# Performance work log

Hardware: AMD Instinct MI355X
Metric: run time of the kernel (lower is better)

Reference implementation:

```python
import jax, jax.numpy as jnp
import numpy as np

# ---- static configuration (mirrors init_kwargs) ----
B, V, C, NH, HD = 1, 6, 256, 8, 32     # batch, views, embed, heads, head_dim
Z, L, P = 4, 4, 2                       # z-ref points, fmap levels, ref points
BEV_H, BEV_W = 80, 80
Q = BEV_H * BEV_W
IMG_H, IMG_W = 480, 800
LEVEL_SHAPES = [(60, 100), (30, 50), (15, 25), (8, 13)]
S = sum(h * w for h, w in LEVEL_SHAPES)
RES = 0.512
OFFSET_SCALE = 1.0
FF = 512


def layer_norm(x, g, b):
    m = jnp.mean(x, -1, keepdims=True)
    v = jnp.var(x, -1, keepdims=True)
    return (x - m) / jnp.sqrt(v + 1e-5) * g + b


def _bev_grid():
    xs = (jnp.arange(BEV_W) + 0.5) / BEV_W
    ys = (jnp.arange(BEV_H) + 0.5) / BEV_H
    gy, gx = jnp.meshgrid(ys, xs, indexing='ij')
    ref = jnp.stack([gx.reshape(-1), gy.reshape(-1)], -1)        # (Q,2) normalized xy
    world = (ref - 0.5) * jnp.array([BEV_W * RES, BEV_H * RES])  # (Q,2) ego-frame meters
    return ref, world


def deform_sample(value, H, W, loc):
    """Bilinear sampling. value: (N, H*W, NH, HD); loc: (N, Qn, NH, PP, 2) in [0,1].
    Returns (N, Qn, NH, PP, HD); out-of-bounds samples contribute zero."""
    v = jnp.moveaxis(value, 2, 1)                                # (N, NH, HW, HD)
    x = loc[..., 0] * W - 0.5
    y = loc[..., 1] * H - 0.5
    x0 = jnp.floor(x); y0 = jnp.floor(y)
    lx, ly = x - x0, y - y0
    x0 = x0.astype(jnp.int32); y0 = y0.astype(jnp.int32)
    gather = jax.vmap(jax.vmap(lambda vt, it: vt[it]))           # over (N, NH)
    def corner(xi, yi, w):
        ok = ((xi >= 0) & (xi < W) & (yi >= 0) & (yi < H)).astype(value.dtype)
        idx = jnp.clip(yi, 0, H - 1) * W + jnp.clip(xi, 0, W - 1)
        g = gather(v, jnp.moveaxis(idx, 2, 1))                   # (N,NH,Qn,PP,HD)
        return jnp.moveaxis(g, 1, 2) * (w * ok)[..., None]
    return (corner(x0, y0, (1 - lx) * (1 - ly)) + corner(x0 + 1, y0, lx * (1 - ly))
            + corner(x0, y0 + 1, (1 - lx) * ly) + corner(x0 + 1, y0 + 1, lx * ly))


def _forward(bev_queries, bev_histories, multiscale_fmaps, transition_matrices, z_refs,
             cam_proj_matrices, Wv_t, Woff_t, boff_t, Ww_t, bw_t, Wo_t, bo_t, ln1_g, ln1_b,
             Wv_s, Woff_s, boff_s, Ww_s, bw_s, Wo_s, bo_s, ln2_g, ln2_b,
             W1, b1, W2, b2, ln3_g, ln3_b):
    ref, world = _bev_grid()
    q = bev_queries
    # ---------- temporal self-attention (deformable over current + warped history) ----------
    vcur = (q @ Wv_t).reshape(B, Q, NH, HD)
    vhist = (bev_histories @ Wv_t).reshape(B, Q, NH, HD)
    off_t = (q @ Woff_t + boff_t).reshape(B, Q, NH, 2, P, 2) * OFFSET_SCALE
    w_t = jax.nn.softmax((q @ Ww_t + bw_t).reshape(B, Q, NH, 2 * P), -1).reshape(B, Q, NH, 2, P)
    ext = jnp.array([BEV_W * RES, BEV_H * RES], jnp.float32)
    wh = jnp.concatenate([world, jnp.ones((Q, 1), jnp.float32)], -1)     # (Q,3)
    warped = jnp.einsum('bij,qj->bqi', transition_matrices, wh)          # (B,Q,3)
    ref_hist = warped[..., :2] / warped[..., 2:3] / ext + 0.5            # (B,Q,2)
    norm_bev = jnp.array([BEV_W, BEV_H], jnp.float32)
    loc_c = ref[None, :, None, None, :] + off_t[:, :, :, 0] / norm_bev
    loc_h = ref_hist[:, :, None, None, :] + off_t[:, :, :, 1] / norm_bev
    s_c = deform_sample(vcur, BEV_H, BEV_W, loc_c)                       # (B,Q,NH,P,HD)
    s_h = deform_sample(vhist, BEV_H, BEV_W, loc_h)
    out_t = (jnp.einsum('bqhp,bqhpd->bqhd', w_t[:, :, :, 0], s_c)
             + jnp.einsum('bqhp,bqhpd->bqhd', w_t[:, :, :, 1], s_h))
    out1 = out_t.reshape(B, Q, C) @ Wo_t + bo_t
    out2 = layer_norm(out1 + q, ln1_g, ln1_b)
    # ---------- spatial cross-attention (multi-view multi-scale deformable) ----------
    val = (multiscale_fmaps @ Wv_s).reshape(B * V, S, NH, HD)
    pts = jnp.concatenate([
        jnp.broadcast_to(world[:, None, :], (Q, Z, 2)),
        jnp.broadcast_to(z_refs[None, :, None], (Q, Z, 1)),
        jnp.ones((Q, Z, 1), jnp.float32)], -1)                           # (Q,Z,4) homogeneous
    uvd = jnp.einsum('vij,qzj->vqzi', cam_proj_matrices, pts)            # (V,Q,Z,3)
    d = uvd[..., 2]
    un = uvd[..., 0] / jnp.maximum(d, 1e-5) / IMG_W
    vn = uvd[..., 1] / jnp.maximum(d, 1e-5) / IMG_H
    valid = ((d > 1e-5) & (un >= 0) & (un <= 1) & (vn >= 0) & (vn <= 1)).astype(q.dtype)
    refuv = jnp.stack([un, vn], -1)                                      # (V,Q,Z,2)
    off_s = (out2 @ Woff_s + boff_s).reshape(B, Q, NH, Z, L, P, 2) * OFFSET_SCALE
    w_s = jax.nn.softmax((out2 @ Ww_s + bw_s).reshape(B, Q, NH, Z * L * P), -1)
    w_s = w_s.reshape(B, Q, NH, Z, L, P)
    acc = jnp.zeros((B, Q, NH, HD), q.dtype)
    start = 0
    for l, (Hl, Wl) in enumerate(LEVEL_SHAPES):
        vl = val[:, start:start + Hl * Wl]
        start += Hl * Wl
        loc = (refuv[None, :, :, None, :, None, :]
               + off_s[:, None, :, :, :, l] / jnp.array([Wl, Hl], jnp.float32))
        loc = jnp.broadcast_to(loc, (B, V, Q, NH, Z, P, 2)).reshape(B * V, Q, NH, Z * P, 2)
        samp = deform_sample(vl, Hl, Wl, loc).reshape(B, V, Q, NH, Z, P, HD)
        wl = w_s[:, None, :, :, :, l] * valid[None, :, :, None, :, None]
        acc = acc + jnp.einsum('bvqhzp,bvqhzpd->bqhd', wl, samp)
    count = jnp.maximum(valid.sum((0, 2)), 1.0)                          # (Q,) hit count
    out3 = (acc / count[None, :, None, None]).reshape(B, Q, C) @ Wo_s + bo_s
    out4 = layer_norm(out3 + out2, ln2_g, ln2_b)
    # ---------- feed-forward ----------
    out5 = jax.nn.relu(out4 @ W1 + b1) @ W2 + b2
    return layer_norm(out5 + out4, ln3_g, ln3_b)


def setup_inputs() -> dict:
    key = jax.random.key(0)
    ks = iter(jax.random.split(key, 40))
    def rn(shape, s=1.0):
        return jax.random.normal(next(ks), shape, jnp.float32) * s
    sc = 1.0 / float(np.sqrt(C))
    inp = {}
    inp['bev_queries'] = rn((B, Q, C), 0.1)
    inp['bev_histories'] = rn((B, Q, C), 0.1)
    inp['multiscale_fmaps'] = rn((B, V, S, C), 0.1)
    th = 0.02
    T = np.array([[np.cos(th), -np.sin(th), 0.5],
                  [np.sin(th), np.cos(th), 0.1],
                  [0.0, 0.0, 1.0]], np.float32)
    inp['transition_matrices'] = jnp.tile(jnp.asarray(T)[None], (B, 1, 1))
    inp['z_refs'] = jnp.linspace(-5.0, 3.0, Z).astype(jnp.float32)
    K = np.array([[400.0, 0.0, IMG_W / 2], [0.0, 400.0, IMG_H / 2], [0.0, 0.0, 1.0]], np.float32)
    Ps = []
    for vi in range(V):
        a = 2 * np.pi * vi / V
        Rt = np.zeros((3, 4), np.float32)
        Rt[0, :3] = [-np.sin(a), np.cos(a), 0.0]   # camera right
        Rt[1, :3] = [0.0, 0.0, -1.0]               # camera down
        Rt[2, :3] = [np.cos(a), np.sin(a), 0.0]    # camera forward
        Ps.append(K @ Rt)
    inp['cam_proj_matrices'] = jnp.asarray(np.stack(Ps))
    # temporal self-attention params
    inp['Wv_t'] = rn((C, C), sc)
    inp['Woff_t'] = rn((C, NH * 2 * P * 2), sc * 0.1)
    inp['boff_t'] = jnp.zeros((NH * 2 * P * 2,), jnp.float32)
    inp['Ww_t'] = rn((C, NH * 2 * P), sc)
    inp['bw_t'] = jnp.zeros((NH * 2 * P,), jnp.float32)
    inp['Wo_t'] = rn((C, C), sc)
    inp['bo_t'] = jnp.zeros((C,), jnp.float32)
    inp['ln1_g'] = jnp.ones((C,), jnp.float32)
    inp['ln1_b'] = jnp.zeros((C,), jnp.float32)
    # spatial cross-attention params
    inp['Wv_s'] = rn((C, C), sc)
    inp['Woff_s'] = rn((C, NH * Z * L * P * 2), sc * 0.1)
    inp['boff_s'] = jnp.zeros((NH * Z * L * P * 2,), jnp.float32)
    inp['Ww_s'] = rn((C, NH * Z * L * P), sc)
    inp['bw_s'] = jnp.zeros((NH * Z * L * P,), jnp.float32)
    inp['Wo_s'] = rn((C, C), sc)
    inp['bo_s'] = jnp.zeros((C,), jnp.float32)
    inp['ln2_g'] = jnp.ones((C,), jnp.float32)
    inp['ln2_b'] = jnp.zeros((C,), jnp.float32)
    # FFN params
    inp['W1'] = rn((C, FF), sc)
    inp['b1'] = jnp.zeros((FF,), jnp.float32)
    inp['W2'] = rn((FF, C), 1.0 / float(np.sqrt(FF)))
    inp['b2'] = jnp.zeros((C,), jnp.float32)
    inp['ln3_g'] = jnp.ones((C,), jnp.float32)
    inp['ln3_b'] = jnp.zeros((C,), jnp.float32)
    # static shape descriptors (treated as compile-time constants)
    inp['bev_spatial_shape'] = np.array([[BEV_H, BEV_W]], np.int64)
    inp['multiscale_fmap_shapes'] = np.array(LEVEL_SHAPES, np.int64)
    inp['img_spatial_shape'] = np.array([[IMG_H, IMG_W]], np.int64)
    return inp


def reference(bev_queries, bev_histories, multiscale_fmaps, transition_matrices, z_refs,
              cam_proj_matrices, Wv_t, Woff_t, boff_t, Ww_t, bw_t, Wo_t, bo_t, ln1_g, ln1_b,
              Wv_s, Woff_s, boff_s, Ww_s, bw_s, Wo_s, bo_s, ln2_g, ln2_b,
              W1, b1, W2, b2, ln3_g, ln3_b,
              bev_spatial_shape, multiscale_fmap_shapes, img_spatial_shape):
    return _forward(bev_queries, bev_histories, multiscale_fmaps, transition_matrices, z_refs,
                    cam_proj_matrices, Wv_t, Woff_t, boff_t, Ww_t, bw_t, Wo_t, bo_t, ln1_g, ln1_b,
                    Wv_s, Woff_s, boff_s, Ww_s, bw_s, Wo_s, bo_s, ln2_g, ln2_b,
                    W1, b1, W2, b2, ln3_g, ln3_b)
```

## Files before the change

kernel.cpp:

```cpp
#include <hip/hip_runtime.h>
#include <hip/hip_bf16.h>
#include <hip/hip_fp16.h>

typedef unsigned short u16;
typedef unsigned int u32;
typedef __attribute__((ext_vector_type(8))) short bf16x8;
typedef __attribute__((ext_vector_type(4))) float f32x4;

#define Q_N  6400
#define S_N  7979
#define BEV  80

__device__ __forceinline__ float ubf(u16 u) {
    return __uint_as_float(((u32)u) << 16);
}
__device__ __forceinline__ u16 bfrn(float x) {
    u32 b = __float_as_uint(x);
    return (u16)((b + 0x7FFFu + ((b >> 16) & 1u)) >> 16);
}
__device__ __forceinline__ float f16tof(u16 u) {
    __half h; *(u16*)&h = u; return __half2float(h);
}
__device__ __forceinline__ u16 ftof16(float f) {
    __half h = __float2half(f); return *(u16*)&h;
}

template <int AIN, int RELU, int OUTMODE, int SM4, int SM32>
__device__ __forceinline__ void gemm_body(
    const void* __restrict__ A, const u16* __restrict__ WhT, const u16* __restrict__ WlT,
    const float* __restrict__ bias, const float* __restrict__ bias2,
    void* __restrict__ Cout, int M, int N, int K, int bx, int by,
    u16* Ah, u16* Al, u16* Wh, u16* Wl)
{
    const int tid  = threadIdx.x;
    const int lane = tid & 63;
    const int wave = tid >> 6;
    const int wm = (wave >> 1) * 32, wn = (wave & 1) * 64;
    const int m0 = by * 64, n0 = bx * 128;
    const int arow = tid >> 2, ak = (tid & 3) * 8;
    const int wrow = tid >> 1, wk = (tid & 1) * 16;
    const int fr = lane & 15, g = lane >> 4;

    f32x4 acc[8];
    #pragma unroll
    for (int i = 0; i < 8; ++i) acc[i] = (f32x4)(0.f);

    for (int k0 = 0; k0 < K; k0 += 32) {
        {
            const bool okr = (m0 + arow) < M;
            float vals[8];
            if (AIN == 0) {
                const float* ap = (const float*)A + (size_t)(m0 + arow) * K + k0 + ak;
                float4 v0 = okr ? *(const float4*)(ap)     : make_float4(0.f, 0.f, 0.f, 0.f);
                float4 v1 = okr ? *(const float4*)(ap + 4) : make_float4(0.f, 0.f, 0.f, 0.f);
                vals[0] = v0.x; vals[1] = v0.y; vals[2] = v0.z; vals[3] = v0.w;
                vals[4] = v1.x; vals[5] = v1.y; vals[6] = v1.z; vals[7] = v1.w;
            } else {
                const u16* ap = (const u16*)A + (size_t)(m0 + arow) * K + k0 + ak;
                uint4 u = okr ? *(const uint4*)ap : make_uint4(0, 0, 0, 0);
                const __half2* hp = (const __half2*)&u;
                #pragma unroll
                for (int i = 0; i < 4; ++i) {
                    float2 f = __half22float2(hp[i]);
                    vals[2 * i] = f.x; vals[2 * i + 1] = f.y;
                }
            }
            u16 hb[8], lb[8];
            #pragma unroll
            for (int i = 0; i < 8; ++i) {
                hb[i] = bfrn(vals[i]);
                lb[i] = bfrn(vals[i] - ubf(hb[i]));
            }
            u16* dh = &Ah[arow * 40 + ak];
            u16* dl = &Al[arow * 40 + ak];
            *(ushort4*)(dh)     = *(ushort4*)&hb[0];
            *(ushort4*)(dh + 4) = *(ushort4*)&hb[4];
            *(ushort4*)(dl)     = *(ushort4*)&lb[0];
            *(ushort4*)(dl + 4) = *(ushort4*)&lb[4];
        }
        {
            const size_t wo = (size_t)(n0 + wrow) * K + k0 + wk;
            *(uint4*)&Wh[wrow * 40 + wk]     = *(const uint4*)(WhT + wo);
            *(uint4*)&Wh[wrow * 40 + wk + 8] = *(const uint4*)(WhT + wo + 8);
            *(uint4*)&Wl[wrow * 40 + wk]     = *(const uint4*)(WlT + wo);
            *(uint4*)&Wl[wrow * 40 + wk + 8] = *(const uint4*)(WlT + wo + 8);
        }
        __syncthreads();
        bf16x8 fah[2], fal[2], fwh[4], fwl[4];
        #pragma unroll
        for (int i = 0; i < 2; ++i) {
            fah[i] = *(const bf16x8*)&Ah[(wm + i * 16 + fr) * 40 + g * 8];
            fal[i] = *(const bf16x8*)&Al[(wm + i * 16 + fr) * 40 + g * 8];
        }
        #pragma unroll
        for (int j = 0; j < 4; ++j) {
            fwh[j] = *(const bf16x8*)&Wh[(wn + j * 16 + fr) * 40 + g * 8];
            fwl[j] = *(const bf16x8*)&Wl[(wn + j * 16 + fr) * 40 + g * 8];
        }
        #pragma unroll
        for (int i = 0; i < 2; ++i)
            #pragma unroll
            for (int j = 0; j < 4; ++j) {
                acc[i * 4 + j] = __builtin_amdgcn_mfma_f32_16x16x32_bf16(fah[i], fwh[j], acc[i * 4 + j], 0, 0, 0);
                acc[i * 4 + j] = __builtin_amdgcn_mfma_f32_16x16x32_bf16(fal[i], fwh[j], acc[i * 4 + j], 0, 0, 0);
                acc[i * 4 + j] = __builtin_amdgcn_mfma_f32_16x16x32_bf16(fah[i], fwl[j], acc[i * 4 + j], 0, 0, 0);
            }
        __syncthreads();
    }
    const int g4r = g * 4;
    float bv[4];
    #pragma unroll
    for (int j = 0; j < 4; ++j) {
        int col = n0 + wn + j * 16 + fr;
        if (bias2) bv[j] = (col < 512) ? bias[col] : bias2[col - 512];
        else       bv[j] = bias ? bias[col] : 0.f;
    }
    const bool do_sm32 = SM32 && ((n0 + wn) >= 512);
    const bool do_sm4  = SM4 && (wn == 64);
    #pragma unroll
    for (int i = 0; i < 2; ++i) {
        #pragma unroll
        for (int r = 0; r < 4; ++r) {
            const int row = m0 + wm + i * 16 + g4r + r;
            float v0 = acc[i * 4 + 0][r] + bv[0];
            float v1 = acc[i * 4 + 1][r] + bv[1];
            float v2 = acc[i * 4 + 2][r] + bv[2];
            float v3 = acc[i * 4 + 3][r] + bv[3];
            if (RELU) {
                v0 = fmaxf(v0, 0.f); v1 = fmaxf(v1, 0.f);
                v2 = fmaxf(v2, 0.f); v3 = fmaxf(v3, 0.f);
            }
            if (SM4 && do_sm4) {
                float m0q = fmaxf(v0, __shfl_xor(v0, 1));
                m0q = fmaxf(m0q, __shfl_xor(m0q, 2));
                float e0 = __expf(v0 - m0q);
                float s0 = e0 + __shfl_xor(e0, 1);
                s0 += __shfl_xor(s0, 2);
                v0 = e0 / s0;
                float m1q = fmaxf(v1, __shfl_xor(v1, 1));
                m1q = fmaxf(m1q, __shfl_xor(m1q, 2));
                float e1 = __expf(v1 - m1q);
                float s1 = e1 + __shfl_xor(e1, 1);
                s1 += __shfl_xor(s1, 2);
                v1 = e1 / s1;
                v2 = 0.f; v3 = 0.f;
            }
            if (SM32 && do_sm32) {
                float ma = fmaxf(v0, v1);
                ma = fmaxf(ma, __shfl_xor(ma, 1));
                ma = fmaxf(ma, __shfl_xor(ma, 2));
                ma = fmaxf(ma, __shfl_xor(ma, 4));
                ma = fmaxf(ma, __shfl_xor(ma, 8));
                float e0 = __expf(v0 - ma), e1 = __expf(v1 - ma);
                float sa = e0 + e1;
                sa += __shfl_xor(sa, 1);
                sa += __shfl_xor(sa, 2);
                sa += __shfl_xor(sa, 4);
                sa += __shfl_xor(sa, 8);
                float ia = 1.f / sa;
                v0 = e0 * ia; v1 = e1 * ia;
                float mb = fmaxf(v2, v3);
                mb = fmaxf(mb, __shfl_xor(mb, 1));
                mb = fmaxf(mb, __shfl_xor(mb, 2));
                mb = fmaxf(mb, __shfl_xor(mb, 4));
                mb = fmaxf(mb, __shfl_xor(mb, 8));
                float e2 = __expf(v2 - mb), e3 = __expf(v3 - mb);
                float sb = e2 + e3;
                sb += __shfl_xor(sb, 1);
                sb += __shfl_xor(sb, 2);
                sb += __shfl_xor(sb, 4);
                sb += __shfl_xor(sb, 8);
                float ib = 1.f / sb;
                v2 = e2 * ib; v3 = e3 * ib;
            }
            if (row < M) {
                const int colb = n0 + wn + fr;
                if (OUTMODE == 1) {
                    u16* cp = (u16*)Cout + (size_t)row * N;
                    cp[colb]      = ftof16(v0);
                    cp[colb + 16] = ftof16(v1);
                    cp[colb + 32] = ftof16(v2);
                    cp[colb + 48] = ftof16(v3);
                } else {
                    float* cp = (float*)Cout + (size_t)row * N;
                    cp[colb]      = v0;
                    cp[colb + 16] = v1;
                    cp[colb + 32] = v2;
                    cp[colb + 48] = v3;
                }
            }
        }
    }
}

template <int AIN, int RELU, int OUTMODE, int SM32>
__global__ __launch_bounds__(256) void mgemm_k(
    const void* __restrict__ A, const u16* __restrict__ WhT, const u16* __restrict__ WlT,
    const float* __restrict__ bias, const float* __restrict__ bias2,
    void* __restrict__ Cout, int M, int N, int K)
{
    __shared__ u16 Ah[64 * 40], Al[64 * 40], Wh[128 * 40], Wl[128 * 40];
    gemm_body<AIN, RELU, OUTMODE, 0, SM32>(A, WhT, WlT, bias, bias2, Cout,
                                           M, N, K, blockIdx.x, blockIdx.y, Ah, Al, Wh, Wl);
}

__global__ __launch_bounds__(256) void fused3_k(
    const float* __restrict__ fmaps, const float* __restrict__ q, const float* __restrict__ hist,
    const u16* __restrict__ Wv_s_h, const u16* __restrict__ Wv_s_l,
    const u16* __restrict__ Wv_t_h, const u16* __restrict__ Wv_t_l,
    const u16* __restrict__ Wc_h,   const u16* __restrict__ Wc_l,
    const float* __restrict__ bc,
    u16* __restrict__ val_f16, u16* __restrict__ vcur, u16* __restrict__ vhist,
    float* __restrict__ owt)
{
    __shared__ u16 Ah[64 * 40], Al[64 * 40], Wh[128 * 40], Wl[128 * 40];
    const int b = blockIdx.x;
    if (b < 1498) {
        gemm_body<0, 0, 1, 0, 0>(fmaps, Wv_s_h, Wv_s_l, nullptr, nullptr, val_f16,
                                 47874, 256, 256, b & 1, b >> 1, Ah, Al, Wh, Wl);
    } else if (b < 1698) {
        int l = b - 1498;
        gemm_body<0, 0, 1, 0, 0>(q, Wv_t_h, Wv_t_l, nullptr, nullptr, vcur,
                                 6400, 256, 256, l & 1, l >> 1, Ah, Al, Wh, Wl);
    } else if (b < 1898) {
        int l = b - 1698;
        gemm_body<0, 0, 1, 0, 0>(hist, Wv_t_h, Wv_t_l, nullptr, nullptr, vhist,
                                 6400, 256, 256, l & 1, l >> 1, Ah, Al, Wh, Wl);
    } else {
        int l = b - 1898;
        gemm_body<0, 0, 0, 1, 0>(q, Wc_h, Wc_l, bc, nullptr, owt,
                                 6400, 128, 256, 0, l, Ah, Al, Wh, Wl);
    }
}

__global__ __launch_bounds__(256) void wprep_k(
    const float* __restrict__ w0, const float* __restrict__ w1, const float* __restrict__ w2,
    const float* __restrict__ w3, const float* __restrict__ w4, const float* __restrict__ w5,
    const float* __restrict__ w6, const float* __restrict__ w7, u16* __restrict__ base,
    const float* __restrict__ Woff_t, const float* __restrict__ Ww_t,
    const float* __restrict__ boff_t, const float* __restrict__ bw_t,
    float* __restrict__ bc)
{
    const int b = blockIdx.x, tid = threadIdx.x;
    if (b == 184) {
        if (tid < 128) bc[tid] = (tid < 64) ? boff_t[tid] : (tid < 96 ? bw_t[tid - 64] : 0.f);
        return;
    }
    const int cum[10]  = {0, 16, 32, 48, 80, 96, 112, 144, 176, 184};
    const int Ks[9]    = {256, 256, 256, 256, 256, 256, 256, 512, 256};
    const int Ns[9]    = {256, 256, 256, 512, 256, 256, 512, 256, 128};
    const int hoff[9]  = {0, 131072, 262144, 393216, 524288, 786432, 917504, 1179648, 1441792};
    const int loff[9]  = {65536, 196608, 327680, 589824, 720896, 851968, 1048576, 1310720, 1474560};
    int seg = 0;
    #pragma unroll
    for (int s = 1; s < 9; ++s) if (b >= cum[s]) seg = s;
    const int K = Ks[seg], N = Ns[seg];
    const int t = b - cum[seg];
    const int ntn = N / 64;
    const int k0 = (t / ntn) * 64, n0 = (t % ntn) * 64;
    __shared__ float tile[64][65];
    const int rr = tid >> 2, cc = (tid & 3) * 16;
    if (seg < 8) {
        const float* W = seg == 0 ? w0 : seg == 1 ? w1 : seg == 2 ? w2 : seg == 3 ? w3 :
                         seg == 4 ? w4 : seg == 5 ? w5 : seg == 6 ? w6 : w7;
        #pragma unroll
        for (int c = 0; c < 4; ++c) {
            float4 v = *(const float4*)(W + (size_t)(k0 + rr) * N + n0 + cc + c * 4);
            tile[rr][cc + c * 4 + 0] = v.x;
            tile[rr][cc + c * 4 + 1] = v.y;
            tile[rr][cc + c * 4 + 2] = v.z;
            tile[rr][cc + c * 4 + 3] = v.w;
        }
    } else {
        #pragma unroll
        for (int i = 0; i < 16; ++i) {
            int n = n0 + cc + i, k = k0 + rr;
            float v = (n < 64) ? Woff_t[k * 64 + n] : (n < 96 ? Ww_t[k * 32 + n - 64] : 0.f);
            tile[rr][cc + i] = v;
        }
    }
    __syncthreads();
    const int nr = tid >> 2, kc = (tid & 3) * 16;
    u16 hb[16], lb[16];
    #pragma unroll
    for (int i = 0; i < 16; ++i) {
        float v = tile[kc + i][nr];
        hb[i] = bfrn(v);
        lb[i] = bfrn(v - ubf(hb[i]));
    }
    u16* hp = base + hoff[seg] + (size_t)(n0 + nr) * K + k0 + kc;
    u16* lp = base + loff[seg] + (size_t)(n0 + nr) * K + k0 + kc;
    *(ushort4*)(hp + 0)  = *(ushort4*)&hb[0];
    *(ushort4*)(hp + 4)  = *(ushort4*)&hb[4];
    *(ushort4*)(hp + 8)  = *(ushort4*)&hb[8];
    *(ushort4*)(hp + 12) = *(ushort4*)&hb[12];
    *(ushort4*)(lp + 0)  = *(ushort4*)&lb[0];
    *(ushort4*)(lp + 4)  = *(ushort4*)&lb[4];
    *(ushort4*)(lp + 8)  = *(ushort4*)&lb[8];
    *(ushort4*)(lp + 12) = *(ushort4*)&lb[12];
}

__global__ __launch_bounds__(256) void ln_k(
    const float* __restrict__ x, const float* __restrict__ res,
    const float* __restrict__ g, const float* __restrict__ b,
    float* __restrict__ out)
{
    const int row = blockIdx.x, t = threadIdx.x;
    const size_t idx = (size_t)row * 256 + t;
    float v = x[idx] + res[idx];
    float s = v, ss = v * v;
    #pragma unroll
    for (int o = 32; o > 0; o >>= 1) {
        s += __shfl_down(s, o);
        ss += __shfl_down(ss, o);
    }
    __shared__ float red[8];
    __shared__ float mv[2];
    const int wv = t >> 6, ln = t & 63;
    if (ln == 0) { red[wv] = s; red[4 + wv] = ss; }
    __syncthreads();
    if (t == 0) {
        float S = red[0] + red[1] + red[2] + red[3];
        float SS = red[4] + red[5] + red[6] + red[7];
        float mean = S * (1.f / 256.f);
        float var = SS * (1.f / 256.f) - mean * mean;
        mv[0] = mean;
        mv[1] = rsqrtf(var + 1e-5f);
    }
    __syncthreads();
    out[idx] = (v - mv[0]) * mv[1] * g[t] + b[t];
}

__device__ __forceinline__ float4 bilin4h(const u16* __restrict__ v, int H, int W,
                                          float x, float y, int chb)
{
    float xf = floorf(x), yf = floorf(y);
    int x0 = (int)xf, y0 = (int)yf;
    int x1 = x0 + 1, y1 = y0 + 1;
    float fx = x - xf, fy = y - yf;
    float w00 = (1.f - fx) * (1.f - fy), w10 = fx * (1.f - fy);
    float w01 = (1.f - fx) * fy,         w11 = fx * fy;
    bool xi0 = (x0 >= 0) && (x0 < W);
    bool xi1 = (x1 >= 0) && (x1 < W);
    bool yi0 = (y0 >= 0) && (y0 < H);
    bool yi1 = (y1 >= 0) && (y1 < H);
    float4 r = make_float4(0.f, 0.f, 0.f, 0.f);
    #define CORNER(xi, yi, xx, yy, ww)                                           \
        if ((yi) && (xi)) {                                                      \
            uint2 u = *(const uint2*)(v + ((size_t)(yy) * W + (xx)) * 256 + chb);\
            float2 f0 = __half22float2(*(const __half2*)&u.x);                   \
            float2 f1 = __half22float2(*(const __half2*)&u.y);                   \
            r.x += (ww) * f0.x; r.y += (ww) * f0.y;                              \
            r.z += (ww) * f1.x; r.w += (ww) * f1.y;                              \
        }
    CORNER(xi0, yi0, x0, y0, w00)
    CORNER(xi1, yi0, x1, y0, w10)
    CORNER(xi0, yi1, x0, y1, w01)
    CORNER(xi1, yi1, x1, y1, w11)
    #undef CORNER
    return r;
}

__global__ __launch_bounds__(256) void temporal_k(
    const u16* __restrict__ vcur, const u16* __restrict__ vhist,
    const float* __restrict__ ow,
    const float* __restrict__ Tm, float* __restrict__ outt)
{
    const int b = blockIdx.x;
    const int q = (b & 7) * 800 + (b >> 3);
    const int tid = threadIdx.x;
    const int c4 = tid & 63, rep = tid >> 6;
    const int br = rep >> 1, p = rep & 1;
    const int h = c4 >> 3;
    const int chb = h * 32 + (c4 & 7) * 4;
    const int jx = q % BEV, iy = q / BEV;
    const float refx = (jx + 0.5f) / 80.f;
    const float refy = (iy + 0.5f) / 80.f;
    const float wx = (refx - 0.5f) * 40.96f;
    const float wy = (refy - 0.5f) * 40.96f;
    float bx, by;
    const u16* v;
    if (br == 0) { v = vcur; bx = refx; by = refy; }
    else {
        float h0 = Tm[0] * wx + Tm[1] * wy + Tm[2];
        float h1 = Tm[3] * wx + Tm[4] * wy + Tm[5];
        float h2 = Tm[6] * wx + Tm[7] * wy + Tm[8];
        v = vhist;
        bx = h0 / h2 / 40.96f + 0.5f;
        by = h1 / h2 / 40.96f + 0.5f;
    }
    const float* owq = ow + (size_t)q * 128;
    int ob = h * 8 + br * 4 + p * 2;
    float lx = bx + owq[ob] * (1.f / 80.f);
    float ly = by + owq[ob + 1] * (1.f / 80.f);
    float wgt = owq[64 + h * 4 + br * 2 + p];
    float4 sv = bilin4h(v, BEV, BEV, lx * 80.f - 0.5f, ly * 80.f - 0.5f, chb);
    __shared__ float4 s_acc[4][64];
    s_acc[rep][c4] = make_float4(wgt * sv.x, wgt * sv.y, wgt * sv.z, wgt * sv.w);
    __syncthreads();
    if (rep == 0) {
        float4 a = s_acc[0][c4], b2 = s_acc[1][c4], c = s_acc[2][c4], d = s_acc[3][c4];
        float4 o = make_float4(a.x + b2.x + c.x + d.x, a.y + b2.y + c.y + d.y,
                               a.z + b2.z + c.z + d.z, a.w + b2.w + c.w + d.w);
        *(float4*)(outt + (size_t)q * 256 + c4 * 4) = o;
    }
}

__global__ __launch_bounds__(256) void spatial_k(
    const u16* __restrict__ val, const u16* __restrict__ ow,
    const float* __restrict__ cam, const float* __restrict__ zrefs,
    float* __restrict__ out)
{
    const int b = blockIdx.x;
    const int q = (b & 7) * 800 + (b >> 3);
    const int tid = threadIdx.x;
    const int lane = tid & 63, wave = tid >> 6;
    const int hw = lane >> 5, lh = lane & 31;
    const int slot = wave * 2 + hw;
    const int h = lh >> 2, chb = h * 32 + (lh & 3) * 8;
    __shared__ float s_un[24], s_vn[24], s_ok[24];
    __shared__ int s_list[24];
    __shared__ int s_n;
    __shared__ float s_cnt;
    __shared__ float s_ox[256], s_oy[256], s_wt[256];
    __shared__ float s_part[8][256];
    const int jx = q % BEV, iy = q / BEV;
    const float wx = ((jx + 0.5f) / 80.f - 0.5f) * 40.96f;
    const float wy = ((iy + 0.5f) / 80.f - 0.5f) * 40.96f;
    if (tid < 24) {
        int v = tid >> 2, zz = tid & 3;
        float zr = zrefs[zz];
        const float* P = cam + v * 12;
        float u0 = P[0] * wx + P[1] * wy + P[2] * zr + P[3];
        float u1 = P[4] * wx + P[5] * wy + P[6] * zr + P[7];
        float dd = P[8] * wx + P[9] * wy + P[10] * zr + P[11];
        float dm = fmaxf(dd, 1e-5f);
        float un = u0 / dm / 800.f;
        float vn = u1 / dm / 480.f;
        bool ok = (dd > 1e-5f) && (un >= 0.f) && (un <= 1.f) && (vn >= 0.f) && (vn <= 1.f);
        s_un[tid] = un; s_vn[tid] = vn; s_ok[tid] = ok ? 1.f : 0.f;
    }
    {
        const u16* owq = ow + (size_t)q * 768;
        #pragma unroll
        for (int rep = 0; rep < 2; ++rep) {
            int flat = tid + rep * 256;
            int hh = flat >> 6, rem = flat & 63;
            int zz = rem >> 4, ll = (rem >> 2) & 3, pp = (rem >> 1) & 1, xy = rem & 1;
            int dst = (zz * 8 + ll * 2 + pp) * 8 + hh;
            float v = f16tof(owq[flat]);
            if (xy) s_oy[dst] = v; else s_ox[dst] = v;
        }
        int hh = tid >> 5, rem = tid & 31;
        s_wt[rem * 8 + hh] = f16tof(owq[512 + tid]);
    }
    __syncthreads();
    if (tid == 0) {
        int n = 0; float c = 0.f;
        for (int vz = 0; vz < 24; ++vz) {
            if (s_ok[vz] != 0.f) { s_list[n++] = vz; c += 1.f; }
        }
        s_n = n; s_cnt = fmaxf(c, 1.f);
    }
    __syncthreads();
    const int n = s_n;
    const int LH[4] = {60, 30, 15, 8};
    const int LW[4] = {100, 50, 25, 13};
    const int LS[4] = {0, 6000, 7500, 7875};
    float a0 = 0.f, a1 = 0.f, a2 = 0.f, a3 = 0.f, a4 = 0.f, a5 = 0.f, a6 = 0.f, a7 = 0.f;
    for (int it = slot; it < n; it += 8) {
        int vz = s_list[it];
        int v = vz >> 2, z = vz & 3;
        float un = s_un[vz], vn = s_vn[vz];
        #pragma unroll
        for (int l = 0; l < 4; ++l) {
            const int Hl = LH[l], Wl = LW[l];
            const u16* lv = val + ((size_t)v * S_N + LS[l]) * 256 + chb;
            const float unl = un * Wl - 0.5f, vnl = vn * Hl - 0.5f;
            #pragma unroll
            for (int p = 0; p < 2; ++p) {
                int idx = (z * 8 + l * 2 + p) * 8 + h;
                float x = unl + s_ox[idx];
                float y = vnl + s_oy[idx];
                float wgt = s_wt[idx];
                float xf = floorf(x), yf = floorf(y);
                int x0 = (int)xf, y0 = (int)yf;
                float fx = x - xf, fy = y - yf;
                __half2 w00 = __float2half2_rn((1.f - fx) * (1.f - fy) * wgt);
                __half2 w10 = __float2half2_rn(fx * (1.f - fy) * wgt);
                __half2 w01 = __float2half2_rn((1.f - fx) * fy * wgt);
                __half2 w11 = __float2half2_rn(fx * fy * wgt);
                bool xi0 = (x0 >= 0) && (x0 < Wl);
                bool xi1 = (x0 + 1 >= 0) && (x0 + 1 < Wl);
                bool yi0 = (y0 >= 0) && (y0 < Hl);
                bool yi1 = (y0 + 1 >= 0) && (y0 + 1 < Hl);
                const u16* r0p = lv + (size_t)y0 * (Wl * 256);
                const u16* r1p = r0p + (size_t)(Wl * 256);
                __half2 h0 = __float2half2_rn(0.f), h1 = h0, h2 = h0, h3 = h0;
                if (yi0 && xi0) {
                    uint4 u = *(const uint4*)(r0p + (size_t)x0 * 256);
                    const __half2* hp = (const __half2*)&u;
                    h0 = __hfma2(w00, hp[0], h0); h1 = __hfma2(w00, hp[1], h1);
                    h2 = __hfma2(w00, hp[2], h2); h3 = __hfma2(w00, hp[3], h3);
                }
                if (yi0 && xi1) {
                    uint4 u = *(const uint4*)(r0p + (size_t)(x0 + 1) * 256);
                    const __half2* hp = (const __half2*)&u;
                    h0 = __hfma2(w10, hp[0], h0); h1 = __hfma2(w10, hp[1], h1);
                    h2 = __hfma2(w10, hp[2], h2); h3 = __hfma2(w10, hp[3], h3);
                }
                if (yi1 && xi0) {
                    uint4 u = *(const uint4*)(r1p + (size_t)x0 * 256);
                    const __half2* hp = (const __half2*)&u;
                    h0 = __hfma2(w01, hp[0], h0); h1 = __hfma2(w01, hp[1], h1);
                    h2 = __hfma2(w01, hp[2], h2); h3 = __hfma2(w01, hp[3], h3);
                }
                if (yi1 && xi1) {
                    uint4 u = *(const uint4*)(r1p + (size_t)(x0 + 1) * 256);
                    const __half2* hp = (const __half2*)&u;
                    h0 = __hfma2(w11, hp[0], h0); h1 = __hfma2(w11, hp[1], h1);
                    h2 = __hfma2(w11, hp[2], h2); h3 = __hfma2(w11, hp[3], h3);
                }
                float2 f0 = __half22float2(h0), f1 = __half22float2(h1);
                float2 f2 = __half22float2(h2), f3 = __half22float2(h3);
                a0 += f0.x; a1 += f0.y; a2 += f1.x; a3 += f1.y;
                a4 += f2.x; a5 += f2.y; a6 += f3.x; a7 += f3.y;
            }
        }
    }
    *(float4*)&s_part[slot][chb]     = make_float4(a0, a1, a2, a3);
    *(float4*)&s_part[slot][chb + 4] = make_float4(a4, a5, a6, a7);
    __syncthreads();
    float sum = 0.f;
    #pragma unroll
    for (int k = 0; k < 8; ++k) sum += s_part[k][tid];
    out[(size_t)q * 256 + tid] = sum / s_cnt;
}

extern "C" void kernel_launch(void* const* d_in, const int* in_sizes, int n_in,
                              void* d_out, int out_size, void* d_ws, size_t ws_size,
                              hipStream_t stream) {
    (void)in_sizes; (void)n_in; (void)out_size; (void)ws_size;
    const float* q      = (const float*)d_in[0];
    const float* hist   = (const float*)d_in[1];
    const float* fmaps  = (const float*)d_in[2];
    const float* Tm     = (const float*)d_in[3];
    const float* zrefs  = (const float*)d_in[4];
    const float* cam    = (const float*)d_in[5];
    const float* Woff_t = (const float*)d_in[7];
    const float* boff_t = (const float*)d_in[8];
    const float* Ww_t   = (const float*)d_in[9];
    const float* bw_t   = (const float*)d_in[10];
    const float* bo_t   = (const float*)d_in[12];
    const float* ln1g   = (const float*)d_in[13];
    const float* ln1b   = (const float*)d_in[14];
    const float* boff_s = (const float*)d_in[17];
    const float* bw_s   = (const float*)d_in[19];
    const float* bo_s   = (const float*)d_in[21];
    const float* ln2g   = (const float*)d_in[22];
    const float* ln2b   = (const float*)d_in[23];
    const float* b1     = (const float*)d_in[25];
    const float* b2     = (const float*)d_in[27];
    const float* ln3g   = (const float*)d_in[28];
    const float* ln3b   = (const float*)d_in[29];

    float* ws    = (float*)d_ws;
    float* r0    = ws;
    float* r1    = ws + 1638400;
    float* owt   = ws + 3276800;
    float* r4    = ws + 4096000;
    u16*  r5u    = (u16*)(ws + 5734400);
    float* of4   = ws + 8192000;
    u16*  valbuf = (u16*)(ws + 9830400);
    u16*  vcur   = (u16*)(ws + 15958272);
    u16*  vhist  = (u16*)(ws + 16777472);
    u16*  wtab   = (u16*)(ws + 17596672);
    float* bc    = ws + 18350336;

    u16* hidden = valbuf;
    u16* Wv_t_h = wtab + 0,       *Wv_t_l = wtab + 65536;
    u16* Wo_t_h = wtab + 131072,  *Wo_t_l = wtab + 196608;
    u16* Wv_s_h = wtab + 262144,  *Wv_s_l = wtab + 327680;
    u16* Comb_h = wtab + 393216,  *Comb_l = wtab + 589824;
    u16* Wo_s_h = wtab + 786432,  *Wo_s_l = wtab + 851968;
    u16* W1_h   = wtab + 917504,  *W1_l   = wtab + 1048576;
    u16* W2_h   = wtab + 1179648, *W2_l   = wtab + 1310720;
    u16* Wc_h   = wtab + 1441792, *Wc_l   = wtab + 1474560;

    dim3 blk(256);
    auto gm = [](int M, int N) { return dim3((unsigned)(N / 128), (unsigned)((M + 63) / 64)); };

    wprep_k<<<dim3(185), blk, 0, stream>>>(
        (const float*)d_in[6], (const float*)d_in[11], (const float*)d_in[15],
        (const float*)d_in[16], (const float*)d_in[18], (const float*)d_in[20],
        (const float*)d_in[24], (const float*)d_in[26], wtab,
        Woff_t, Ww_t, boff_t, bw_t, bc);
    fused3_k<<<dim3(1998), blk, 0, stream>>>(
        fmaps, q, hist, Wv_s_h, Wv_s_l, Wv_t_h, Wv_t_l, Wc_h, Wc_l, bc,
        valbuf, vcur, vhist, owt);
    temporal_k<<<dim3(6400), blk, 0, stream>>>(vcur, vhist, owt, Tm, r4);
    mgemm_k<0,0,0,0><<<gm(6400, 256), blk, 0, stream>>>(
        r4, Wo_t_h, Wo_t_l, bo_t, nullptr, r0, 6400, 256, 256);
    ln_k<<<dim3(6400), blk, 0, stream>>>(r0, q, ln1g, ln1b, r1);
    mgemm_k<0,0,1,1><<<gm(6400, 768), blk, 0, stream>>>(
        r1, Comb_h, Comb_l, boff_s, bw_s, r5u, 6400, 768, 256);
    spatial_k<<<dim3(6400), blk, 0, stream>>>(valbuf, r5u, cam, zrefs, r0);
    mgemm_k<0,0,0,0><<<gm(6400, 256), blk, 0, stream>>>(
        r0, Wo_s_h, Wo_s_l, bo_s, nullptr, r4, 6400, 256, 256);
    ln_k<<<dim3(6400), blk, 0, stream>>>(r4, r1, ln2g, ln2b, of4);
    mgemm_k<0,1,1,0><<<gm(6400, 512), blk, 0, stream>>>(
        of4, W1_h, W1_l, b1, nullptr, hidden, 6400, 512, 256);
    mgemm_k<1,0,0,0><<<gm(6400, 256), blk, 0, stream>>>(
        hidden, W2_h, W2_l, b2, nullptr, r0, 6400, 256, 512);
    ln_k<<<dim3(6400), blk, 0, stream>>>(r0, of4, ln3g, ln3b, (float*)d_out);
}
```

Measured before the change: 351.2 us.

## Use 64x256 GEMM tiles for value projections and split spatial sampling by level

Adds a gemm_body256 variant where each block computes a full 256-wide output tile, so every A row is loaded and split into bf16 hi/lo once instead of twice. This halves the fused3_k block count and removes the redundant A reads and conversions, at the cost of more shared memory (about 50 KB) and twice the accumulators per thread, which may lower occupancy. The spatial sampling loop now gives each slot one (view,z,level) item instead of a (view,z) pair covering all four levels, spreading the work more evenly across the 8 slots.

```diff
diff --git a/kernel.cpp b/kernel.cpp
--- a/kernel.cpp
+++ b/kernel.cpp
@@ -39,7 +39,7 @@
     const int m0 = by * 64, n0 = bx * 128;
     const int arow = tid >> 2, ak = (tid & 3) * 8;
     const int wrow = tid >> 1, wk = (tid & 1) * 16;
-    const int fr = lane & 15, g = lane >> 4;
+    const int fr = lane & 15, gq = lane >> 4;
 
     f32x4 acc[8];
     #pragma unroll
@@ -71,12 +71,10 @@
                 hb[i] = bfrn(vals[i]);
                 lb[i] = bfrn(vals[i] - ubf(hb[i]));
             }
-            u16* dh = &Ah[arow * 40 + ak];
-            u16* dl = &Al[arow * 40 + ak];
-            *(ushort4*)(dh)     = *(ushort4*)&hb[0];
-            *(ushort4*)(dh + 4) = *(ushort4*)&hb[4];
-            *(ushort4*)(dl)     = *(ushort4*)&lb[0];
-            *(ushort4*)(dl + 4) = *(ushort4*)&lb[4];
+            *(ushort4*)(&Ah[arow * 40 + ak])     = *(ushort4*)&hb[0];
+            *(ushort4*)(&Ah[arow * 40 + ak + 4]) = *(ushort4*)&hb[4];
+            *(ushort4*)(&Al[arow * 40 + ak])     = *(ushort4*)&lb[0];
+            *(ushort4*)(&Al[arow * 40 + ak + 4]) = *(ushort4*)&lb[4];
         }
         {
             const size_t wo = (size_t)(n0 + wrow) * K + k0 + wk;
@@ -89,13 +87,13 @@
         bf16x8 fah[2], fal[2], fwh[4], fwl[4];
         #pragma unroll
         for (int i = 0; i < 2; ++i) {
-            fah[i] = *(const bf16x8*)&Ah[(wm + i * 16 + fr) * 40 + g * 8];
-            fal[i] = *(const bf16x8*)&Al[(wm + i * 16 + fr) * 40 + g * 8];
+            fah[i] = *(const bf16x8*)&Ah[(wm + i * 16 + fr) * 40 + gq * 8];
+            fal[i] = *(const bf16x8*)&Al[(wm + i * 16 + fr) * 40 + gq * 8];
         }
         #pragma unroll
         for (int j = 0; j < 4; ++j) {
-            fwh[j] = *(const bf16x8*)&Wh[(wn + j * 16 + fr) * 40 + g * 8];
-            fwl[j] = *(const bf16x8*)&Wl[(wn + j * 16 + fr) * 40 + g * 8];
+            fwh[j] = *(const bf16x8*)&Wh[(wn + j * 16 + fr) * 40 + gq * 8];
+            fwl[j] = *(const bf16x8*)&Wl[(wn + j * 16 + fr) * 40 + gq * 8];
         }
         #pragma unroll
         for (int i = 0; i < 2; ++i)
@@ -107,7 +105,7 @@
             }
         __syncthreads();
     }
-    const int g4r = g * 4;
+    const int g4r = gq * 4;
     float bv[4];
     #pragma unroll
     for (int j = 0; j < 4; ++j) {
@@ -193,15 +191,122 @@
     }
 }
 
+template <int AIN, int OUTMODE>
+__device__ __forceinline__ void gemm_body256(
+    const void* __restrict__ A, const u16* __restrict__ WhT, const u16* __restrict__ WlT,
+    const float* __restrict__ bias, void* __restrict__ Cout, int M, int K, int by, u16* smem)
+{
+    u16* Ah = smem;
+    u16* Al = smem + 2560;
+    u16* Wh = smem + 5120;
+    u16* Wl = smem + 15360;
+    const int tid  = threadIdx.x;
+    const int lane = tid & 63;
+    const int wave = tid >> 6;
+    const int wm = (wave >> 1) * 32, wn = (wave & 1) * 128;
+    const int m0 = by * 64;
+    const int arow = tid >> 2, ak = (tid & 3) * 8;
+    const int fr = lane & 15, gq = lane >> 4;
+
+    f32x4 acc[16];
+    #pragma unroll
+    for (int i = 0; i < 16; ++i) acc[i] = (f32x4)(0.f);
+
+    for (int k0 = 0; k0 < K; k0 += 32) {
+        {
+            const bool okr = (m0 + arow) < M;
+            float vals[8];
+            if (AIN == 0) {
+                const float* ap = (const float*)A + (size_t)(m0 + arow) * K + k0 + ak;
+                float4 v0 = okr ? *(const float4*)(ap)     : make_float4(0.f, 0.f, 0.f, 0.f);
+                float4 v1 = okr ? *(const float4*)(ap + 4) : make_float4(0.f, 0.f, 0.f, 0.f);
+                vals[0] = v0.x; vals[1] = v0.y; vals[2] = v0.z; vals[3] = v0.w;
+                vals[4] = v1.x; vals[5] = v1.y; vals[6] = v1.z; vals[7] = v1.w;
+            } else {
+                const u16* ap = (const u16*)A + (size_t)(m0 + arow) * K + k0 + ak;
+                uint4 u = okr ? *(const uint4*)ap : make_uint4(0, 0, 0, 0);
+                const __half2* hp = (const __half2*)&u;
+                #pragma unroll
+                for (int i = 0; i < 4; ++i) {
+                    float2 f = __half22float2(hp[i]);
+                    vals[2 * i] = f.x; vals[2 * i + 1] = f.y;
+                }
+            }
+            u16 hb[8], lb[8];
+            #pragma unroll
+            for (int i = 0; i < 8; ++i) {
+                hb[i] = bfrn(vals[i]);
+                lb[i] = bfrn(vals[i] - ubf(hb[i]));
+            }
+            *(ushort4*)(&Ah[arow * 40 + ak])     = *(ushort4*)&hb[0];
+            *(ushort4*)(&Ah[arow * 40 + ak + 4]) = *(ushort4*)&hb[4];
+            *(ushort4*)(&Al[arow * 40 + ak])     = *(ushort4*)&lb[0];
+            *(ushort4*)(&Al[arow * 40 + ak + 4]) = *(ushort4*)&lb[4];
+        }
+        {
+            const size_t wo = (size_t)tid * K + k0;
+            const uint4* sh = (const uint4*)(WhT + wo);
+            const uint4* sl = (const uint4*)(WlT + wo);
+            uint4* dh = (uint4*)&Wh[tid * 40];
+            uint4* dl = (uint4*)&Wl[tid * 40];
+            dh[0] = sh[0]; dh[1] = sh[1]; dh[2] = sh[2]; dh[3] = sh[3];
+            dl[0] = sl[0]; dl[1] = sl[1]; dl[2] = sl[2]; dl[3] = sl[3];
+        }
+        __syncthreads();
+        bf16x8 fah[2], fal[2];
+        #pragma unroll
+        for (int i = 0; i < 2; ++i) {
+            fah[i] = *(const bf16x8*)&Ah[(wm + i * 16 + fr) * 40 + gq * 8];
+            fal[i] = *(const bf16x8*)&Al[(wm + i * 16 + fr) * 40 + gq * 8];
+        }
+        #pragma unroll
+        for (int jg = 0; jg < 2; ++jg) {
+            bf16x8 fwh[4], fwl[4];
+            #pragma unroll
+            for (int j = 0; j < 4; ++j) {
+                fwh[j] = *(const bf16x8*)&Wh[(wn + jg * 64 + j * 16 + fr) * 40 + gq * 8];
+                fwl[j] = *(const bf16x8*)&Wl[(wn + jg * 64 + j * 16 + fr) * 40 + gq * 8];
+            }
+            #pragma unroll
+            for (int i = 0; i < 2; ++i)
+                #pragma unroll
+                for (int j = 0; j < 4; ++j) {
+                    int a = i * 8 + jg * 4 + j;
+                    acc[a] = __builtin_amdgcn_mfma_f32_16x16x32_bf16(fah[i], fwh[j], acc[a], 0, 0, 0);
+                    acc[a] = __builtin_amdgcn_mfma_f32_16x16x32_bf16(fal[i], fwh[j], acc[a], 0, 0, 0);
+                    acc[a] = __builtin_amdgcn_mfma_f32_16x16x32_bf16(fah[i], fwl[j], acc[a], 0, 0, 0);
+                }
+        }
+        __syncthreads();
+    }
+    const int g4r = gq * 4;
+    #pragma unroll
+    for (int i = 0; i < 2; ++i) {
+        #pragma unroll
+        for (int r = 0; r < 4; ++r) {
+            const int row = m0 + wm + i * 16 + g4r + r;
+            if (row >= M) continue;
+            #pragma unroll
+            for (int j = 0; j < 8; ++j) {
+                int col = wn + j * 16 + fr;
+                float v = acc[i * 8 + j][r] + (bias ? bias[col] : 0.f);
+                if (OUTMODE == 1) ((u16*)Cout)[(size_t)row * 256 + col] = ftof16(v);
+                else              ((float*)Cout)[(size_t)row * 256 + col] = v;
+            }
+        }
+    }
+}
+
 template <int AIN, int RELU, int OUTMODE, int SM32>
 __global__ __launch_bounds__(256) void mgemm_k(
     const void* __restrict__ A, const u16* __restrict__ WhT, const u16* __restrict__ WlT,
     const float* __restrict__ bias, const float* __restrict__ bias2,
     void* __restrict__ Cout, int M, int N, int K)
 {
-    __shared__ u16 Ah[64 * 40], Al[64 * 40], Wh[128 * 40], Wl[128 * 40];
+    __shared__ u16 smem[15360];
     gemm_body<AIN, RELU, OUTMODE, 0, SM32>(A, WhT, WlT, bias, bias2, Cout,
-                                           M, N, K, blockIdx.x, blockIdx.y, Ah, Al, Wh, Wl);
+                                           M, N, K, blockIdx.x, blockIdx.y,
+                                           smem, smem + 2560, smem + 5120, smem + 10240);
 }
 
 __global__ __launch_bounds__(256) void fused3_k(
@@ -213,23 +318,18 @@
     u16* __restrict__ val_f16, u16* __restrict__ vcur, u16* __restrict__ vhist,
     float* __restrict__ owt)
 {
-    __shared__ u16 Ah[64 * 40], Al[64 * 40], Wh[128 * 40], Wl[128 * 40];
+    __shared__ u16 smem[25600];
     const int b = blockIdx.x;
-    if (b < 1498) {
-        gemm_body<0, 0, 1, 0, 0>(fmaps, Wv_s_h, Wv_s_l, nullptr, nullptr, val_f16,
-                                 47874, 256, 256, b & 1, b >> 1, Ah, Al, Wh, Wl);
-    } else if (b < 1698) {
-        int l = b - 1498;
-        gemm_body<0, 0, 1, 0, 0>(q, Wv_t_h, Wv_t_l, nullptr, nullptr, vcur,
-                                 6400, 256, 256, l & 1, l >> 1, Ah, Al, Wh, Wl);
-    } else if (b < 1898) {
-        int l = b - 1698;
-        gemm_body<0, 0, 1, 0, 0>(hist, Wv_t_h, Wv_t_l, nullptr, nullptr, vhist,
-                                 6400, 256, 256, l & 1, l >> 1, Ah, Al, Wh, Wl);
+    if (b < 749) {
+        gemm_body256<0, 1>(fmaps, Wv_s_h, Wv_s_l, nullptr, val_f16, 47874, 256, b, smem);
+    } else if (b < 849) {
+        gemm_body256<0, 1>(q, Wv_t_h, Wv_t_l, nullptr, vcur, 6400, 256, b - 749, smem);
+    } else if (b < 949) {
+        gemm_body256<0, 1>(hist, Wv_t_h, Wv_t_l, nullptr, vhist, 6400, 256, b - 849, smem);
     } else {
-        int l = b - 1898;
         gemm_body<0, 0, 0, 1, 0>(q, Wc_h, Wc_l, bc, nullptr, owt,
-                                 6400, 128, 256, 0, l, Ah, Al, Wh, Wl);
+                                 6400, 128, 256, 0, b - 949,
+                                 smem, smem + 2560, smem + 5120, smem + 10240);
     }
 }
 
@@ -363,8 +463,7 @@
 
 __global__ __launch_bounds__(256) void temporal_k(
     const u16* __restrict__ vcur, const u16* __restrict__ vhist,
-    const float* __restrict__ ow,
-    const float* __restrict__ Tm, float* __restrict__ outt)
+    const float* __restrict__ ow, const float* __restrict__ Tm, float* __restrict__ outt)
 {
     const int b = blockIdx.x;
     const int q = (b & 7) * 800 + (b >> 3);
@@ -425,15 +524,15 @@
     __shared__ float s_ox[256], s_oy[256], s_wt[256];
     __shared__ float s_part[8][256];
     const int jx = q % BEV, iy = q / BEV;
-    const float wx = ((jx + 0.5f) / 80.f - 0.5f) * 40.96f;
-    const float wy = ((iy + 0.5f) / 80.f - 0.5f) * 40.96f;
+    const float wxw = ((jx + 0.5f) / 80.f - 0.5f) * 40.96f;
+    const float wyw = ((iy + 0.5f) / 80.f - 0.5f) * 40.96f;
     if (tid < 24) {
         int v = tid >> 2, zz = tid & 3;
         float zr = zrefs[zz];
         const float* P = cam + v * 12;
-        float u0 = P[0] * wx + P[1] * wy + P[2] * zr + P[3];
-        float u1 = P[4] * wx + P[5] * wy + P[6] * zr + P[7];
-        float dd = P[8] * wx + P[9] * wy + P[10] * zr + P[11];
+        float u0 = P[0] * wxw + P[1] * wyw + P[2] * zr + P[3];
+        float u1 = P[4] * wxw + P[5] * wyw + P[6] * zr + P[7];
+        float dd = P[8] * wxw + P[9] * wyw + P[10] * zr + P[11];
         float dm = fmaxf(dd, 1e-5f);
         float un = u0 / dm / 800.f;
         float vn = u1 / dm / 480.f;
@@ -463,69 +562,66 @@
         s_n = n; s_cnt = fmaxf(c, 1.f);
     }
     __syncthreads();
-    const int n = s_n;
+    const int nu = s_n * 4;
     const int LH[4] = {60, 30, 15, 8};
     const int LW[4] = {100, 50, 25, 13};
     const int LS[4] = {0, 6000, 7500, 7875};
     float a0 = 0.f, a1 = 0.f, a2 = 0.f, a3 = 0.f, a4 = 0.f, a5 = 0.f, a6 = 0.f, a7 = 0.f;
-    for (int it = slot; it < n; it += 8) {
-        int vz = s_list[it];
-        int v = vz >> 2, z = vz & 3;
-        float un = s_un[vz], vn = s_vn[vz];
-        #pragma unroll
-        for (int l = 0; l < 4; ++l) {
-            const int Hl = LH[l], Wl = LW[l];
-            const u16* lv = val + ((size_t)v * S_N + LS[l]) * 256 + chb;
-            const float unl = un * Wl - 0.5f, vnl = vn * Hl - 0.5f;
-            #pragma unroll
-            for (int p = 0; p < 2; ++p) {
-                int idx = (z * 8 + l * 2 + p) * 8 + h;
-                float x = unl + s_ox[idx];
-                float y = vnl + s_oy[idx];
-                float wgt = s_wt[idx];
-                float xf = floorf(x), yf = floorf(y);
-                int x0 = (int)xf, y0 = (int)yf;
-                float fx = x - xf, fy = y - yf;
-                __half2 w00 = __float2half2_rn((1.f - fx) * (1.f - fy) * wgt);
-                __half2 w10 = __float2half2_rn(fx * (1.f - fy) * wgt);
-                __half2 w01 = __float2half2_rn((1.f - fx) * fy * wgt);
-                __half2 w11 = __float2half2_rn(fx * fy * wgt);
-                bool xi0 = (x0 >= 0) && (x0 < Wl);
-                bool xi1 = (x0 + 1 >= 0) && (x0 + 1 < Wl);
-                bool yi0 = (y0 >= 0) && (y0 < Hl);
-                bool yi1 = (y0 + 1 >= 0) && (y0 + 1 < Hl);
-                const u16* r0p = lv + (size_t)y0 * (Wl * 256);
-                const u16* r1p = r0p + (size_t)(Wl * 256);
-                __half2 h0 = __float2half2_rn(0.f), h1 = h0, h2 = h0, h3 = h0;
-                if (yi0 && xi0) {
-                    uint4 u = *(const uint4*)(r0p + (size_t)x0 * 256);
-                    const __half2* hp = (const __half2*)&u;
-                    h0 = __hfma2(w00, hp[0], h0); h1 = __hfma2(w00, hp[1], h1);
-                    h2 = __hfma2(w00, hp[2], h2); h3 = __hfma2(w00, hp[3], h3);
-                }
-                if (yi0 && xi1) {
-                    uint4 u = *(const uint4*)(r0p + (size_t)(x0 + 1) * 256);
-                    const __half2* hp = (const __half2*)&u;
-                    h0 = __hfma2(w10, hp[0], h0); h1 = __hfma2(w10, hp[1], h1);
-                    h2 = __hfma2(w10, hp[2], h2); h3 = __hfma2(w10, hp[3], h3);
-                }
-                if (yi1 && xi0) {
-                    uint4 u = *(const uint4*)(r1p + (size_t)x0 * 256);
-                    const __half2* hp = (const __half2*)&u;
-                    h0 = __hfma2(w01, hp[0], h0); h1 = __hfma2(w01, hp[1], h1);
-                    h2 = __hfma2(w01, hp[2], h2); h3 = __hfma2(w01, hp[3], h3);
-                }
-                if (yi1 && xi1) {
-                    uint4 u = *(const uint4*)(r1p + (size_t)(x0 + 1) * 256);
-                    const __half2* hp = (const __half2*)&u;
-                    h0 = __hfma2(w11, hp[0], h0); h1 = __hfma2(w11, hp[1], h1);
-                    h2 = __hfma2(w11, hp[2], h2); h3 = __hfma2(w11, hp[3], h3);
-                }
-                float2 f0 = __half22float2(h0), f1 = __half22float2(h1);
-                float2 f2 = __half22float2(h2), f3 = __half22float2(h3);
-                a0 += f0.x; a1 += f0.y; a2 += f1.x; a3 += f1.y;
-                a4 += f2.x; a5 += f2.y; a6 += f3.x; a7 += f3.y;
-            }
+    for (int it = slot; it < nu; it += 8) {
+        const int vz = s_list[it >> 2];
+        const int l = it & 3;
+        const int v = vz >> 2, z = vz & 3;
+        const int Hl = LH[l], Wl = LW[l];
+        const u16* lv = val + ((size_t)v * S_N + LS[l]) * 256 + chb;
+        const float unl = s_un[vz] * Wl - 0.5f, vnl = s_vn[vz] * Hl - 0.5f;
+        #pragma unroll
+        for (int p = 0; p < 2; ++p) {
+            int idx = (z * 8 + l * 2 + p) * 8 + h;
+            float x = unl + s_ox[idx];
+            float y = vnl + s_oy[idx];
+            float wgt = s_wt[idx];
+            float xf = floorf(x), yf = floorf(y);
+            int x0 = (int)xf, y0 = (int)yf;
+            float fx = x - xf, fy = y - yf;
+            __half2 w00 = __float2half2_rn((1.f - fx) * (1.f - fy) * wgt);
+            __half2 w10 = __float2half2_rn(fx * (1.f - fy) * wgt);
+            __half2 w01 = __float2half2_rn((1.f - fx) * fy * wgt);
+            __half2 w11 = __float2half2_rn(fx * fy * wgt);
+            bool xi0 = (x0 >= 0) && (x0 < Wl);
+            bool xi1 = (x0 + 1 >= 0) && (x0 + 1 < Wl);
+            bool yi0 = (y0 >= 0) && (y0 < Hl);
+            bool yi1 = (y0 + 1 >= 0) && (y0 + 1 < Hl);
+            const u16* r0p = lv + (size_t)y0 * (Wl * 256);
+            const u16* r1p = r0p + (size_t)(Wl * 256);
+            __half2 h0 = __float2half2_rn(0.f), h1 = h0, h2 = h0, h3 = h0;
+            if (yi0 && xi0) {
+                uint4 u = *(const uint4*)(r0p + (size_t)x0 * 256);
+                const __half2* hp = (const __half2*)&u;
+                h0 = __hfma2(w00, hp[0], h0); h1 = __hfma2(w00, hp[1], h1);
+                h2 = __hfma2(w00, hp[2], h2); h3 = __hfma2(w00, hp[3], h3);
+            }
+            if (yi0 && xi1) {
+                uint4 u = *(const uint4*)(r0p + (size_t)(x0 + 1) * 256);
+                const __half2* hp = (const __half2*)&u;
+                h0 = __hfma2(w10, hp[0], h0); h1 = __hfma2(w10, hp[1], h1);
+                h2 = __hfma2(w10, hp[2], h2); h3 = __hfma2(w10, hp[3], h3);
+            }
+            if (yi1 && xi0) {
+                uint4 u = *(const uint4*)(r1p + (size_t)x0 * 256);
+                const __half2* hp = (const __half2*)&u;
+                h0 = __hfma2(w01, hp[0], h0); h1 = __hfma2(w01, hp[1], h1);
+                h2 = __hfma2(w01, hp[2], h2); h3 = __hfma2(w01, hp[3], h3);
+            }
+            if (yi1 && xi1) {
+                uint4 u = *(const uint4*)(r1p + (size_t)(x0 + 1) * 256);
+                const __half2* hp = (const __half2*)&u;
+                h0 = __hfma2(w11, hp[0], h0); h1 = __hfma2(w11, hp[1], h1);
+                h2 = __hfma2(w11, hp[2], h2); h3 = __hfma2(w11, hp[3], h3);
+            }
+            float2 f0 = __half22float2(h0), f1 = __half22float2(h1);
+            float2 f2 = __half22float2(h2), f3 = __half22float2(h3);
+            a0 += f0.x; a1 += f0.y; a2 += f1.x; a3 += f1.y;
+            a4 += f2.x; a5 += f2.y; a6 += f3.x; a7 += f3.y;
         }
     }
     *(float4*)&s_part[slot][chb]     = make_float4(a0, a1, a2, a3);
@@ -595,7 +691,7 @@
         (const float*)d_in[16], (const float*)d_in[18], (const float*)d_in[20],
         (const float*)d_in[24], (const float*)d_in[26], wtab,
         Woff_t, Ww_t, boff_t, bw_t, bc);
-    fused3_k<<<dim3(1998), blk, 0, stream>>>(
+    fused3_k<<<dim3(1049), blk, 0, stream>>>(
         fmaps, q, hist, Wv_s_h, Wv_s_l, Wv_t_h, Wv_t_l, Wc_h, Wc_l, bc,
         valbuf, vcur, vhist, owt);
     temporal_k<<<dim3(6400), blk, 0, stream>>>(vcur, vhist, owt, Tm, r4);
```

Measured after the change: 360.5 us. 1.03x slower.
